# Optimization experiments

Measured on AMD Instinct MI355X. Metric: run time of the kernel, lower is better.

The kernel has to match this reference:

```python
import jax, jax.numpy as jnp
import numpy as np

C = 512
NUM_HEADS = 8
HEAD_DIM = C // NUM_HEADS


def setup_inputs() -> dict:
    key = jax.random.key(0)
    ks = jax.random.split(key, 5)
    B, H, W = 4, 48, 48
    x = jax.random.normal(ks[0], (B, C, H, W), dtype=jnp.float32)
    # 1x1 conv weights == dense matrices over channel dim
    Wqkv = jax.random.normal(ks[1], (3 * C, C), dtype=jnp.float32) * (1.0 / np.sqrt(C))
    bqkv = jax.random.normal(ks[2], (3 * C,), dtype=jnp.float32) * 0.01
    Wout = jax.random.normal(ks[3], (C, C), dtype=jnp.float32) * (1.0 / np.sqrt(C))
    bout = jax.random.normal(ks[4], (C,), dtype=jnp.float32) * 0.01
    return {"x": x, "Wqkv": Wqkv, "bqkv": bqkv, "Wout": Wout, "bout": bout}


def reference(x, Wqkv, bqkv, Wout, bout):
    B, Cc, H, W = x.shape
    S = H * W
    # qkv 1x1 conv: [B, 3C, H, W] -> reshape (B, 3, heads, head_dim, S)
    qkv = jnp.einsum('bchw,oc->bohw', x, Wqkv) + bqkv[None, :, None, None]
    qkv = qkv.reshape(B, 3, NUM_HEADS, HEAD_DIM, S)
    q, k, v = qkv[:, 0], qkv[:, 1], qkv[:, 2]  # [B, h, d, S]
    # tokens along S: q^T k, scaled softmax
    scale = HEAD_DIM ** -0.5
    attn = jnp.einsum('bhds,bhdt->bhst', q, k) * scale  # [B, h, S, S]
    attn = jax.nn.softmax(attn, axis=-1)
    out = jnp.einsum('bhst,bhdt->bhds', attn, v)  # [B, h, d, S]
    out = out.reshape(B, Cc, H, W)
    out = jnp.einsum('bchw,oc->bohw', out, Wout) + bout[None, :, None, None]
    return out
```

## Files before the change

### kernel.cpp

```cpp
#include <hip/hip_runtime.h>

#define S_LEN 2304
#define CDIM  512
#define NHEAD 8

typedef __attribute__((ext_vector_type(4)))  float f32x4;
typedef __attribute__((ext_vector_type(16))) float f32x16;
typedef __attribute__((ext_vector_type(8)))  _Float16 f16x8;
typedef __attribute__((ext_vector_type(2)))  __fp16 fp16x2r;
typedef _Float16 h16;

#define QSCALE 0.18033688011112042f

__device__ __forceinline__ float fexp2(float x) {
#if __has_builtin(__builtin_amdgcn_exp2f)
    return __builtin_amdgcn_exp2f(x);
#else
    return exp2f(x);
#endif
}

__device__ __forceinline__ unsigned cvtpk(float a, float b) {
    union { fp16x2r v; unsigned u; } c;
    c.v = __builtin_amdgcn_cvt_pkrtz(a, b);
    return c.u;
}

__device__ __forceinline__ void gll16(const h16* g, h16* l) {
    __builtin_amdgcn_global_load_lds(
        (const __attribute__((address_space(1))) unsigned int*)g,
        (__attribute__((address_space(3))) unsigned int*)l, 16, 0, 0);
}

__global__ __launch_bounds__(256) void prep(
    const float* __restrict__ x, h16* __restrict__ xT,
    const float* __restrict__ Wq, const float* __restrict__ Wo,
    h16* __restrict__ Wq_h, h16* __restrict__ Wo_h)
{
    const int bid = blockIdx.x;
    if (bid >= 1152) {
        const int NQ = 1536 * 512;
        const int NO = 512 * 512;
        int i = ((bid - 1152) * 256 + threadIdx.x) * 4;
        if (i >= NQ + NO) return;
        float4 v;
        h16* dst;
        if (i < NQ) { v = *(const float4*)(Wq + i);        dst = Wq_h + i; }
        else        { v = *(const float4*)(Wo + (i - NQ)); dst = Wo_h + (i - NQ); }
        union { h16 h[4]; uint2 u; } pk;
        pk.h[0]=(h16)v.x; pk.h[1]=(h16)v.y; pk.h[2]=(h16)v.z; pk.h[3]=(h16)v.w;
        *(uint2*)dst = pk.u;
        return;
    }
    const int s0 = (bid % 36) * 64;
    const int c0 = ((bid / 36) & 7) * 64;
    const int b  = bid / 288;
    __shared__ h16 Ts[64][76];

    const int t  = threadIdx.x;
    const int cq = t >> 4;
    const int sq = t & 15;

    const float* xb = x + ((size_t)b * CDIM + c0 + cq * 4) * S_LEN + s0 + sq * 4;
    float4 r0 = *(const float4*)(xb);
    float4 r1 = *(const float4*)(xb + S_LEN);
    float4 r2 = *(const float4*)(xb + 2 * S_LEN);
    float4 r3 = *(const float4*)(xb + 3 * S_LEN);

    union { h16 h[4]; uint2 u; } pk;
    pk.h[0]=(h16)r0.x; pk.h[1]=(h16)r1.x; pk.h[2]=(h16)r2.x; pk.h[3]=(h16)r3.x;
    *(uint2*)&Ts[sq*4+0][cq*4] = pk.u;
    pk.h[0]=(h16)r0.y; pk.h[1]=(h16)r1.y; pk.h[2]=(h16)r2.y; pk.h[3]=(h16)r3.y;
    *(uint2*)&Ts[sq*4+1][cq*4] = pk.u;
    pk.h[0]=(h16)r0.z; pk.h[1]=(h16)r1.z; pk.h[2]=(h16)r2.z; pk.h[3]=(h16)r3.z;
    *(uint2*)&Ts[sq*4+2][cq*4] = pk.u;
    pk.h[0]=(h16)r0.w; pk.h[1]=(h16)r1.w; pk.h[2]=(h16)r2.w; pk.h[3]=(h16)r3.w;
    *(uint2*)&Ts[sq*4+3][cq*4] = pk.u;

    __syncthreads();
    const int s  = t >> 2;
    const int cc = (t & 3) * 16;
    uint2 a0 = *(uint2*)&Ts[s][cc + 0];
    uint2 a1 = *(uint2*)&Ts[s][cc + 4];
    uint2 a2 = *(uint2*)&Ts[s][cc + 8];
    uint2 a3 = *(uint2*)&Ts[s][cc + 12];
    h16* dst = xT + ((size_t)b * S_LEN + s0 + s) * CDIM + c0 + cc;
    uint4 w0 = make_uint4(a0.x, a0.y, a1.x, a1.y);
    uint4 w1 = make_uint4(a2.x, a2.y, a3.x, a3.y);
    *(uint4*)dst       = w0;
    *(uint4*)(dst + 8) = w1;
}

__global__ __launch_bounds__(256) void gemm_qkv(
    const h16* __restrict__ Wh, const float* __restrict__ bqkv,
    const h16* __restrict__ xT, h16* __restrict__ qT, h16* __restrict__ kT,
    h16* __restrict__ vN)
{
    const int n0 = blockIdx.x * 128;
    const int m0 = blockIdx.y * 128;
    const int b  = blockIdx.z;
    __shared__ h16 Ws[128 * 64];
    __shared__ h16 Xs[128 * 64];

    const int tid = threadIdx.x;
    const int lid = tid & 63, w = tid >> 6;
    const int g = lid >> 4, ln = lid & 15;
    const int wm = w & 1, wn = w >> 1;
    const int srow = lid >> 3;
    const int sblk = (lid & 7) ^ (srow & 7);

    f32x4 acc[4][4];
#pragma unroll
    for (int i = 0; i < 4; i++)
#pragma unroll
        for (int j = 0; j < 4; j++) acc[i][j] = (f32x4)0.f;

    const h16* Wbase = Wh + (size_t)m0 * CDIM;
    const h16* Xbase = xT + ((size_t)b * S_LEN + n0) * CDIM;
    const bool vblk = (m0 >= 1024);

    for (int kt = 0; kt < CDIM; kt += 64) {
        __syncthreads();
#pragma unroll
        for (int i = 0; i < 4; i++) {
            const int row0 = w * 32 + i * 8;
            gll16(Wbase + (size_t)(row0 + srow) * CDIM + kt + sblk * 8, &Ws[row0 * 64]);
            gll16(Xbase + (size_t)(row0 + srow) * CDIM + kt + sblk * 8, &Xs[row0 * 64]);
        }
        __syncthreads();

#pragma unroll
        for (int kc = 0; kc < 2; kc++) {
            f16x8 af[4], bf[4];
#pragma unroll
            for (int i = 0; i < 4; i++) {
                const int ra = wm * 64 + i * 16 + ln;
                const int ca = (kc * 64 + g * 16) ^ ((ra & 7) << 4);
                af[i] = *(const f16x8*)&Ws[ra * 64 + ca / 2];
                const int rb = wn * 64 + i * 16 + ln;
                const int cb = (kc * 64 + g * 16) ^ ((rb & 7) << 4);
                bf[i] = *(const f16x8*)&Xs[rb * 64 + cb / 2];
            }
            if (!vblk) {
#pragma unroll
                for (int i = 0; i < 4; i++)
#pragma unroll
                    for (int j = 0; j < 4; j++)
                        acc[i][j] = __builtin_amdgcn_mfma_f32_16x16x32_f16(
                            af[i], bf[j], acc[i][j], 0, 0, 0);
            } else {
#pragma unroll
                for (int i = 0; i < 4; i++)
#pragma unroll
                    for (int j = 0; j < 4; j++)
                        acc[i][j] = __builtin_amdgcn_mfma_f32_16x16x32_f16(
                            bf[i], af[j], acc[i][j], 0, 0, 0);
            }
        }
    }

    if (!vblk) {
#pragma unroll
        for (int i = 0; i < 4; i++) {
            const int mb = m0 + wm * 64 + i * 16 + 4 * g;
            const float4 bv = *(const float4*)&bqkv[mb];
            const int mloc = mb & 511;
            const int hh = mloc >> 6, d0 = mloc & 63;
            const bool isq = (mb < 512);
            const float scl = isq ? QSCALE : 1.0f;
            h16* base = (isq ? qT : kT);
#pragma unroll
            for (int j = 0; j < 4; j++) {
                const int n = n0 + wn * 64 + j * 16 + ln;
                union { h16 h[4]; uint2 u; } pk;
                pk.h[0] = (h16)((acc[i][j][0] + bv.x) * scl);
                pk.h[1] = (h16)((acc[i][j][1] + bv.y) * scl);
                pk.h[2] = (h16)((acc[i][j][2] + bv.z) * scl);
                pk.h[3] = (h16)((acc[i][j][3] + bv.w) * scl);
                *(uint2*)(base + (((size_t)b * 8 + hh) * S_LEN + n) * 64 + d0) = pk.u;
            }
        }
    } else {
#pragma unroll
        for (int j = 0; j < 4; j++) {
            const int m = m0 + wm * 64 + j * 16 + ln;
            const float bias = bqkv[m];
            const int mloc = m - 1024;
            const int hh = mloc >> 6, d = mloc & 63;
            h16* base = vN + (((size_t)b * 8 + hh) * 64 + d) * S_LEN;
#pragma unroll
            for (int i = 0; i < 4; i++) {
                const int nb = n0 + wn * 64 + i * 16 + 4 * g;
                union { h16 h[4]; uint2 u; } pk;
                pk.h[0] = (h16)(acc[i][j][0] + bias);
                pk.h[1] = (h16)(acc[i][j][1] + bias);
                pk.h[2] = (h16)(acc[i][j][2] + bias);
                pk.h[3] = (h16)(acc[i][j][3] + bias);
                *(uint2*)(base + nb) = pk.u;
            }
        }
    }
}

__global__ __launch_bounds__(256, 3) void attn_f16(
    const h16* __restrict__ qT, const h16* __restrict__ kT,
    const h16* __restrict__ vN, h16* __restrict__ attT)
{
    const int f    = blockIdx.x;
    const int xcd  = f & 7;
    const int slot = f >> 3;
    const int bh   = xcd + 8 * (slot / 18);
    const int x    = slot % 18;
    const int b    = bh >> 3;
    const int h    = bh & 7;
    const int s0   = x * 128;

    __shared__ h16 Ks[3][64 * 64];
    __shared__ h16 Vs[3][64 * 64];

    const int tid = threadIdx.x;
    const int lid = tid & 63, w = tid >> 6;
    const int l31 = lid & 31, hi = lid >> 5;
    const int srow = lid >> 3;
    const int sblk = (lid & 7) ^ (srow & 7);

    const h16* qb = qT + ((size_t)b * 8 + h) * S_LEN * 64;
    const h16* kb = kT + ((size_t)b * 8 + h) * S_LEN * 64;
    const h16* vb = vN + ((size_t)b * 8 + h) * 64 * S_LEN;

    const int sq = s0 + w * 32 + l31;

    f16x8 qf[4];
    {
        const h16* qrow = qb + (size_t)sq * 64;
#pragma unroll
        for (int ds = 0; ds < 4; ds++)
            qf[ds] = *(const f16x8*)(qrow + ds * 16 + hi * 8);
    }

    auto stage = [&](int t, int buf) {
        const int kt = t * 64;
        for (int c = w; c < 16; c += 4) {
            if (c < 8)
                gll16(kb + (size_t)(kt + c * 8 + srow) * 64 + sblk * 8,
                      &Ks[buf][c * 8 * 64]);
            else
                gll16(vb + (size_t)((c - 8) * 8 + srow) * S_LEN + kt + sblk * 8,
                      &Vs[buf][(c - 8) * 8 * 64]);
        }
    };

    stage(0, 0);
    stage(1, 1);
    asm volatile("s_waitcnt vmcnt(4)" ::: "memory");
    __builtin_amdgcn_sched_barrier(0);
    __builtin_amdgcn_s_barrier();
    __builtin_amdgcn_sched_barrier(0);

    float m_run = -1e30f, l_run = 0.f;
    f32x16 oacc0 = (f32x16)0.f, oacc1 = (f32x16)0.f;

    const int NT = S_LEN / 64;
    for (int i = 0; i < NT; i++) {
        const int cur = i % 3;
        if (i + 2 < NT) stage(i + 2, (i + 2) % 3);

        const h16* Kc = Ks[cur];
        const h16* Vc = Vs[cur];

        f32x16 sacc0 = (f32x16)0.f, sacc1 = (f32x16)0.f;
#pragma unroll
        for (int ds = 0; ds < 4; ds++) {
            const int bc = 2 * ds + hi;
            {
                const int row = l31;
                f16x8 kf = *(const f16x8*)&Kc[row * 64 + ((bc ^ (row & 7)) * 8)];
                sacc0 = __builtin_amdgcn_mfma_f32_32x32x16_f16(kf, qf[ds], sacc0, 0, 0, 0);
            }
            {
                const int row = 32 + l31;
                f16x8 kf = *(const f16x8*)&Kc[row * 64 + ((bc ^ (row & 7)) * 8)];
                sacc1 = __builtin_amdgcn_mfma_f32_32x32x16_f16(kf, qf[ds], sacc1, 0, 0, 0);
            }
        }

        float ma = sacc0[0], mb2 = sacc1[0];
#pragma unroll
        for (int r = 1; r < 15; r += 2) {
            ma  = fmaxf(fmaxf(ma,  sacc0[r]), sacc0[r + 1]);
            mb2 = fmaxf(fmaxf(mb2, sacc1[r]), sacc1[r + 1]);
        }
        ma  = fmaxf(ma,  sacc0[15]);
        mb2 = fmaxf(mb2, sacc1[15]);
        float mloc = fmaxf(ma, mb2);
        mloc = fmaxf(mloc, __shfl_xor(mloc, 32));

        if (!__all(mloc <= m_run + 8.0f)) {
            const float mnew = fmaxf(m_run, mloc);
            const float resc = fexp2(m_run - mnew);
#pragma unroll
            for (int r = 0; r < 16; r++) { oacc0[r] *= resc; oacc1[r] *= resc; }
            l_run *= resc;
            m_run = mnew;
        }

        float lsum = 0.f;
#pragma unroll
        for (int r = 0; r < 16; r++) {
            sacc0[r] = fexp2(sacc0[r] - m_run); lsum += sacc0[r];
        }
#pragma unroll
        for (int r = 0; r < 16; r++) {
            sacc1[r] = fexp2(sacc1[r] - m_run); lsum += sacc1[r];
        }
        l_run += lsum + __shfl_xor(lsum, 32);

        f16x8 pf[4];
#pragma unroll
        for (int j = 0; j < 4; j++) {
            const int bse = (j & 1) * 8;
            float pv[8];
#pragma unroll
            for (int r = 0; r < 8; r++)
                pv[r] = (j < 2) ? sacc0[bse + r] : sacc1[bse + r];
            unsigned X0 = cvtpk(pv[0], pv[1]);
            unsigned X1 = cvtpk(pv[2], pv[3]);
            unsigned Y0 = cvtpk(pv[4], pv[5]);
            unsigned Y1 = cvtpk(pv[6], pv[7]);
            asm("v_permlane32_swap_b32 %0, %1" : "+v"(X0), "+v"(Y0));
            asm("v_permlane32_swap_b32 %0, %1" : "+v"(X1), "+v"(Y1));
            union { unsigned u[4]; f16x8 v; } pkk;
            pkk.u[0] = X0; pkk.u[1] = X1; pkk.u[2] = Y0; pkk.u[3] = Y1;
            pf[j] = pkk.v;
        }

#pragma unroll
        for (int j = 0; j < 4; j++) {
            const int bc = 2 * j + hi;
            {
                const int row = l31;
                f16x8 vf = *(const f16x8*)&Vc[row * 64 + ((bc ^ (row & 7)) * 8)];
                oacc0 = __builtin_amdgcn_mfma_f32_32x32x16_f16(vf, pf[j], oacc0, 0, 0, 0);
            }
            {
                const int row = 32 + l31;
                f16x8 vf = *(const f16x8*)&Vc[row * 64 + ((bc ^ (row & 7)) * 8)];
                oacc1 = __builtin_amdgcn_mfma_f32_32x32x16_f16(vf, pf[j], oacc1, 0, 0, 0);
            }
        }

        if (i < NT - 1) {
            if (i + 2 < NT) {
                asm volatile("s_waitcnt vmcnt(4)" ::: "memory");
            } else {
                asm volatile("s_waitcnt vmcnt(0)" ::: "memory");
            }
            __builtin_amdgcn_sched_barrier(0);
            __builtin_amdgcn_s_barrier();
            __builtin_amdgcn_sched_barrier(0);
        }
    }

    const float inv = 1.0f / l_run;
    h16* ob = attT + ((size_t)b * S_LEN + sq) * CDIM + h * 64;
#pragma unroll
    for (int gi = 0; gi < 4; gi++) {
        union { h16 hh[4]; uint2 u; } p0, p1;
#pragma unroll
        for (int r = 0; r < 4; r++) {
            p0.hh[r] = (h16)(oacc0[gi * 4 + r] * inv);
            p1.hh[r] = (h16)(oacc1[gi * 4 + r] * inv);
        }
        *(uint2*)(ob + 8 * gi + 4 * hi)      = p0.u;
        *(uint2*)(ob + 32 + 8 * gi + 4 * hi) = p1.u;
    }
}

__global__ __launch_bounds__(256) void gemm_out(
    const h16* __restrict__ attT, const h16* __restrict__ Wh,
    const float* __restrict__ bout, float* __restrict__ out)
{
    const int n0 = blockIdx.x * 64;
    const int m0 = blockIdx.y * 128;
    const int b  = blockIdx.z;
    __shared__ h16 Ws[128 * 64];
    __shared__ h16 Xs[64 * 64];

    const int tid = threadIdx.x;
    const int lid = tid & 63, w = tid >> 6;
    const int g = lid >> 4, ln = lid & 15;
    const int wm = w & 1, wn = w >> 1;
    const int srow = lid >> 3;
    const int sblk = (lid & 7) ^ (srow & 7);

    f32x4 acc[2][4];
#pragma unroll
    for (int i = 0; i < 2; i++)
#pragma unroll
        for (int j = 0; j < 4; j++) acc[i][j] = (f32x4)0.f;

    const h16* Wbase = Wh + (size_t)m0 * CDIM;
    const h16* Xbase = attT + ((size_t)b * S_LEN + n0) * CDIM;

    for (int kt = 0; kt < CDIM; kt += 64) {
        __syncthreads();
#pragma unroll
        for (int i = 0; i < 4; i++) {
            const int row0 = w * 32 + i * 8;
            gll16(Wbase + (size_t)(row0 + srow) * CDIM + kt + sblk * 8, &Ws[row0 * 64]);
        }
#pragma unroll
        for (int i = 0; i < 2; i++) {
            const int row0 = w * 16 + i * 8;
            if (row0 < 64)
                gll16(Xbase + (size_t)(row0 + srow) * CDIM + kt + sblk * 8, &Xs[row0 * 64]);
        }
        __syncthreads();

#pragma unroll
        for (int kc = 0; kc < 2; kc++) {
            f16x8 af[4], bf[2];
#pragma unroll
            for (int j = 0; j < 4; j++) {
                const int ra = wm * 64 + j * 16 + ln;
                const int ca = (kc * 64 + g * 16) ^ ((ra & 7) << 4);
                af[j] = *(const f16x8*)&Ws[ra * 64 + ca / 2];
            }
#pragma unroll
            for (int i = 0; i < 2; i++) {
                const int rb = wn * 32 + i * 16 + ln;
                const int cb = (kc * 64 + g * 16) ^ ((rb & 7) << 4);
                bf[i] = *(const f16x8*)&Xs[rb * 64 + cb / 2];
            }
#pragma unroll
            for (int i = 0; i < 2; i++)
#pragma unroll
                for (int j = 0; j < 4; j++)
                    acc[i][j] = __builtin_amdgcn_mfma_f32_16x16x32_f16(
                        bf[i], af[j], acc[i][j], 0, 0, 0);
        }
    }

#pragma unroll
    for (int j = 0; j < 4; j++) {
        const int m = m0 + wm * 64 + j * 16 + ln;
        const float bias = bout[m];
        float* base = out + ((size_t)b * CDIM + m) * S_LEN;
#pragma unroll
        for (int i = 0; i < 2; i++) {
            const int nb = n0 + wn * 32 + i * 16 + 4 * g;
            float4 o;
            o.x = acc[i][j][0] + bias;
            o.y = acc[i][j][1] + bias;
            o.z = acc[i][j][2] + bias;
            o.w = acc[i][j][3] + bias;
            *(float4*)(base + nb) = o;
        }
    }
}

extern "C" void kernel_launch(void* const* d_in, const int* in_sizes, int n_in,
                              void* d_out, int out_size, void* d_ws, size_t ws_size,
                              hipStream_t stream)
{
    const float* x    = (const float*)d_in[0];
    const float* Wqkv = (const float*)d_in[1];
    const float* bqkv = (const float*)d_in[2];
    const float* Wout = (const float*)d_in[3];
    const float* bout = (const float*)d_in[4];
    float* out = (float*)d_out;

    h16* xT   = (h16*)d_ws;
    h16* Wq_h = xT   + (size_t)4 * S_LEN * CDIM;
    h16* Wo_h = Wq_h + (size_t)1536 * 512;
    h16* qT   = Wo_h + (size_t)512 * 512;
    h16* kT   = qT   + (size_t)4 * 8 * S_LEN * 64;
    h16* vN   = kT   + (size_t)4 * 8 * S_LEN * 64;
    h16* attT = vN   + (size_t)4 * 8 * S_LEN * 64;

    prep    <<<2176,            256, 0, stream>>>(x, xT, Wqkv, Wout, Wq_h, Wo_h);
    gemm_qkv<<<dim3(18, 12, 4), 256, 0, stream>>>(Wq_h, bqkv, xT, qT, kT, vN);
    attn_f16<<<576,             256, 0, stream>>>(qT, kT, vN, attT);
    gemm_out<<<dim3(36, 4, 4),  256, 0, stream>>>(attT, Wo_h, bout, out);
}
```

Before: 129.2 us.

## Split attention KV range in two halves and merge partials in combine kernel

```diff
diff --git a/kernel.cpp b/kernel.cpp
--- a/kernel.cpp
+++ b/kernel.cpp
@@ -202,21 +202,25 @@
     }
 }
 
-__global__ __launch_bounds__(256, 3) void attn_f16(
+__global__ __launch_bounds__(256, 4) void attn_f16(
     const h16* __restrict__ qT, const h16* __restrict__ kT,
-    const h16* __restrict__ vN, h16* __restrict__ attT)
+    const h16* __restrict__ vN, h16* __restrict__ attT,
+    h16* __restrict__ pO1, float2* __restrict__ pml)
 {
     const int f    = blockIdx.x;
     const int xcd  = f & 7;
     const int slot = f >> 3;
-    const int bh   = xcd + 8 * (slot / 18);
+    const int grp  = slot / 18;
     const int x    = slot % 18;
+    const int bhh  = xcd + 8 * grp;
+    const int bh   = bhh & 31;
+    const int half = bhh >> 5;
     const int b    = bh >> 3;
     const int h    = bh & 7;
     const int s0   = x * 128;
 
-    __shared__ h16 Ks[3][64 * 64];
-    __shared__ h16 Vs[3][64 * 64];
+    __shared__ h16 Ks[2][64 * 64];
+    __shared__ h16 Vs[2][64 * 64];
 
     const int tid = threadIdx.x;
     const int lid = tid & 63, w = tid >> 6;
@@ -224,9 +228,9 @@
     const int srow = lid >> 3;
     const int sblk = (lid & 7) ^ (srow & 7);
 
-    const h16* qb = qT + ((size_t)b * 8 + h) * S_LEN * 64;
-    const h16* kb = kT + ((size_t)b * 8 + h) * S_LEN * 64;
-    const h16* vb = vN + ((size_t)b * 8 + h) * 64 * S_LEN;
+    const h16* qb = qT + ((size_t)bh) * S_LEN * 64;
+    const h16* kb = kT + ((size_t)bh) * S_LEN * 64;
+    const h16* vb = vN + ((size_t)bh) * 64 * S_LEN;
 
     const int sq = s0 + w * 32 + l31;
 
@@ -250,20 +254,16 @@
         }
     };
 
-    stage(0, 0);
-    stage(1, 1);
-    asm volatile("s_waitcnt vmcnt(4)" ::: "memory");
-    __builtin_amdgcn_sched_barrier(0);
-    __builtin_amdgcn_s_barrier();
-    __builtin_amdgcn_sched_barrier(0);
+    const int t0 = half * 18;
+    stage(t0, 0);
+    __syncthreads();
 
     float m_run = -1e30f, l_run = 0.f;
     f32x16 oacc0 = (f32x16)0.f, oacc1 = (f32x16)0.f;
 
-    const int NT = S_LEN / 64;
-    for (int i = 0; i < NT; i++) {
-        const int cur = i % 3;
-        if (i + 2 < NT) stage(i + 2, (i + 2) % 3);
+    for (int i = 0; i < 18; i++) {
+        const int cur = i & 1;
+        if (i + 1 < 18) stage(t0 + i + 1, cur ^ 1);
 
         const h16* Kc = Ks[cur];
         const h16* Vc = Vs[cur];
@@ -348,21 +348,11 @@
                 oacc1 = __builtin_amdgcn_mfma_f32_32x32x16_f16(vf, pf[j], oacc1, 0, 0, 0);
             }
         }
-
-        if (i < NT - 1) {
-            if (i + 2 < NT) {
-                asm volatile("s_waitcnt vmcnt(4)" ::: "memory");
-            } else {
-                asm volatile("s_waitcnt vmcnt(0)" ::: "memory");
-            }
-            __builtin_amdgcn_sched_barrier(0);
-            __builtin_amdgcn_s_barrier();
-            __builtin_amdgcn_sched_barrier(0);
-        }
+        __syncthreads();
     }
 
     const float inv = 1.0f / l_run;
-    h16* ob = attT + ((size_t)b * S_LEN + sq) * CDIM + h * 64;
+    h16* ob = (half ? pO1 : attT) + ((size_t)b * S_LEN + sq) * CDIM + h * 64;
 #pragma unroll
     for (int gi = 0; gi < 4; gi++) {
         union { h16 hh[4]; uint2 u; } p0, p1;
@@ -374,6 +364,38 @@
         *(uint2*)(ob + 8 * gi + 4 * hi)      = p0.u;
         *(uint2*)(ob + 32 + 8 * gi + 4 * hi) = p1.u;
     }
+    if (hi == 0)
+        pml[(size_t)half * 73728 + (size_t)bh * S_LEN + sq] =
+            make_float2(m_run, l_run);
+}
+
+__global__ __launch_bounds__(256) void combine(
+    h16* __restrict__ attT, const h16* __restrict__ pO1,
+    const float2* __restrict__ pml)
+{
+    const int idx8 = (blockIdx.x * 256 + threadIdx.x) * 8;
+    const int b   = idx8 / (S_LEN * CDIM);
+    const int rem = idx8 % (S_LEN * CDIM);
+    const int sq  = rem / CDIM;
+    const int c   = rem % CDIM;
+    const int h   = c >> 6;
+    const size_t row = (size_t)(b * 8 + h) * S_LEN + sq;
+
+    const float2 ml0 = pml[row];
+    const float2 ml1 = pml[73728 + row];
+    const float m  = fmaxf(ml0.x, ml1.x);
+    const float a0 = fexp2(ml0.x - m) * ml0.y;
+    const float a1 = fexp2(ml1.x - m) * ml1.y;
+    const float inv = 1.0f / (a0 + a1);
+    const float w0 = a0 * inv, w1 = a1 * inv;
+
+    union { uint4 u; h16 hh[8]; } x0, x1, o;
+    x0.u = *(const uint4*)(attT + idx8);
+    x1.u = *(const uint4*)(pO1 + idx8);
+#pragma unroll
+    for (int k = 0; k < 8; k++)
+        o.hh[k] = (h16)(w0 * (float)x0.hh[k] + w1 * (float)x1.hh[k]);
+    *(uint4*)(attT + idx8) = o.u;
 }
 
 __global__ __launch_bounds__(256) void gemm_out(
@@ -478,8 +500,12 @@
     h16* vN   = kT   + (size_t)4 * 8 * S_LEN * 64;
     h16* attT = vN   + (size_t)4 * 8 * S_LEN * 64;
 
+    h16*    pO1 = xT;
+    float2* pml = (float2*)Wq_h;
+
     prep    <<<2176,            256, 0, stream>>>(x, xT, Wqkv, Wout, Wq_h, Wo_h);
     gemm_qkv<<<dim3(18, 12, 4), 256, 0, stream>>>(Wq_h, bqkv, xT, qT, kT, vN);
-    attn_f16<<<576,             256, 0, stream>>>(qT, kT, vN, attT);
+    attn_f16<<<1152,            256, 0, stream>>>(qT, kT, vN, attT, pO1, pml);
+    combine <<<2304,            256, 0, stream>>>(attT, pO1, pml);
     gemm_out<<<dim3(36, 4, 4),  256, 0, stream>>>(attT, Wo_h, bout, out);
 }
```

New measurement: 129.0 us. Within noise of the previous version (-0.1%).
